# Kernel optimization log

Hardware: AMD Instinct MI355X
Metric: run time of the kernel (lower is better)

Reference implementation:

```python
import jax, jax.numpy as jnp
import numpy as np

N_HEADS = 8
IN_DIM = 128
H_DIM = 512
B, N, L = 4, 64, 256


def setup_inputs() -> dict:
    key = jax.random.key(0)
    ks = jax.random.split(key, 11)
    s = 0.02
    return {
        "query": jax.random.normal(ks[0], (B, N, L, IN_DIM), jnp.float32),
        "key": jax.random.normal(ks[1], (B, N, L, IN_DIM), jnp.float32),
        "value": jax.random.normal(ks[2], (B, N, L, IN_DIM), jnp.float32),
        "Wq": jax.random.normal(ks[3], (IN_DIM, H_DIM), jnp.float32) * s,
        "bq": jnp.zeros((H_DIM,), jnp.float32),
        "Wk": jax.random.normal(ks[4], (IN_DIM, H_DIM), jnp.float32) * s,
        "bk": jnp.zeros((H_DIM,), jnp.float32),
        "Wv": jax.random.normal(ks[5], (IN_DIM, H_DIM), jnp.float32) * s,
        "bv": jnp.zeros((H_DIM,), jnp.float32),
        "Wo": jax.random.normal(ks[6], (H_DIM, H_DIM), jnp.float32) * s,
        "bo": jnp.zeros((H_DIM,), jnp.float32),
    }


def reference(query, key, value, Wq, bq, Wk, bk, Wv, bv, Wo, bo):
    # Conv2d 1x1 over the channel dim after permute == linear along last dim.
    hd = H_DIM // N_HEADS  # head_dim
    b, n, lq, _ = query.shape
    lk = key.shape[-2]
    q = query @ Wq + bq   # (B, N, Lq, H_DIM)
    k = key @ Wk + bk     # (B, N, Lk, H_DIM)
    v = value @ Wv + bv   # (B, N, Lk, H_DIM)
    # split heads along the last dim (matches torch.split/cat head-major trick)
    q = q.reshape(b, n, lq, N_HEADS, hd)
    k = k.reshape(b, n, lk, N_HEADS, hd)
    v = v.reshape(b, n, lk, N_HEADS, hd)
    scores = jnp.einsum("bnqhd,bnkhd->bnhqk", q, k) / jnp.sqrt(jnp.float32(hd))
    attn = jax.nn.softmax(scores, axis=-1)
    out = jnp.einsum("bnhqk,bnkhd->bnqhd", attn, v).reshape(b, n, lq, H_DIM)
    return out @ Wo + bo
```

## Files before the change

### kernel.cpp

```cpp
#include <hip/hip_runtime.h>
#include <stdint.h>
#include <stddef.h>


typedef __attribute__((ext_vector_type(8))) short short8;
typedef __attribute__((ext_vector_type(4))) float f32x4;

#define AS1(p) ((const __attribute__((address_space(1))) void*)(p))
#define AS3(p) ((__attribute__((address_space(3))) void*)(p))

__device__ __forceinline__ float b2f(uint16_t u) {
    union { uint32_t i; float f; } x; x.i = ((uint32_t)u) << 16; return x.f;
}
__device__ __forceinline__ uint16_t f2b(float f) {
    union { float f; uint32_t i; } x; x.f = f;
    uint32_t r = x.i + 0x7fffu + ((x.i >> 16) & 1u);
    return (uint16_t)(r >> 16);
}

__global__ void k_detect(const uint16_t* __restrict__ q, int* __restrict__ flag) {
    const int t = threadIdx.x;
    int cnt = 0;
    for (int i = 0; i < 32; ++i) {
        const int e = (q[t * 32 + i] >> 7) & 0xff;
        cnt += (e < 110) | (e > 135);
    }
#pragma unroll
    for (int m = 1; m < 64; m <<= 1) cnt += __shfl_xor(cnt, m, 64);
    if (t == 0) *flag = (cnt > 256) ? 1 : 0;
}

__device__ __forceinline__ uint16_t rd_any(const void* p, size_t idx, int isf) {
    return isf ? f2b(((const float*)p)[idx]) : ((const uint16_t*)p)[idx];
}

__global__ void k_transpose(const void* __restrict__ Wq, const void* __restrict__ Wk,
                            const void* __restrict__ Wv, const void* __restrict__ Wo,
                            uint16_t* __restrict__ wtq, uint16_t* __restrict__ wtk,
                            uint16_t* __restrict__ wtv, uint16_t* __restrict__ wto,
                            const int* __restrict__ flag) {
    const int isf = *flag;
    const int z = blockIdx.y;
    const int t = blockIdx.x * 256 + threadIdx.x;
    if (z < 3) {
        if (t >= 128 * 512) return;
        const void* W = (z == 0) ? Wq : (z == 1) ? Wk : Wv;
        uint16_t* o = (z == 0) ? wtq : (z == 1) ? wtk : wtv;
        const int k = t & 127, n = t >> 7;
        o[t] = rd_any(W, (size_t)k * 512 + n, isf);
    } else {
        const int k = t & 511, n = t >> 9;
        wto[t] = rd_any(Wo, (size_t)k * 512 + n, isf);
    }
}

template<int KITERS>
__device__ __forceinline__ void gemm_dev(const void* __restrict__ Av, const int lda,
                                         const uint16_t* __restrict__ Wt,
                                         const void* __restrict__ biasv,
                                         void* __restrict__ Cv,
                                         const int m0, const int n0,
                                         const int isf_a, const int isf_bias, const int isf_c) {
    __shared__ __align__(16) uint16_t At[128 * 64];
    __shared__ __align__(16) uint16_t Bt[128 * 64];
    const int tid = threadIdx.x;
    const int lane = tid & 63, w = tid >> 6;
    const int wr = w >> 1, wc = w & 1;
    const int quad = lane >> 4, cl = lane & 15;

    f32x4 acc[4][4];
#pragma unroll
    for (int i = 0; i < 4; ++i)
#pragma unroll
        for (int j = 0; j < 4; ++j) acc[i][j] = (f32x4){0.f, 0.f, 0.f, 0.f};

#pragma unroll 1
    for (int kt = 0; kt < KITERS; ++kt) {
        const int k0 = kt * 64;
        __syncthreads();
        if (!isf_a) {
#pragma unroll
            for (int i = 0; i < 4; ++i) {
                const int s = i * 256 + tid;
                const int row = s >> 3;
                const int gc = (s & 7) ^ (row & 7);
                __builtin_amdgcn_global_load_lds(AS1((const uint16_t*)Av + (size_t)(m0 + row) * lda + k0 + gc * 8),
                                                 AS3(At + (size_t)(i * 256 + w * 64) * 8), 16, 0, 0);
                __builtin_amdgcn_global_load_lds(AS1(Wt + (size_t)(n0 + row) * lda + k0 + gc * 8),
                                                 AS3(Bt + (size_t)(i * 256 + w * 64) * 8), 16, 0, 0);
            }
        } else {
#pragma unroll
            for (int i = 0; i < 4; ++i) {
                const int s = i * 256 + tid;
                const int row = s >> 3;
                const int gc = (s & 7) ^ (row & 7);
                __builtin_amdgcn_global_load_lds(AS1(Wt + (size_t)(n0 + row) * lda + k0 + gc * 8),
                                                 AS3(Bt + (size_t)(i * 256 + w * 64) * 8), 16, 0, 0);
                const float* p = (const float*)Av + (size_t)(m0 + row) * lda + k0 + gc * 8;
                const f32x4 u0 = *(const f32x4*)p;
                const f32x4 u1 = *(const f32x4*)(p + 4);
                short8 tv;
#pragma unroll
                for (int j = 0; j < 4; ++j) {
                    tv[j] = (short)f2b(u0[j]);
                    tv[4 + j] = (short)f2b(u1[j]);
                }
                *(short8*)(At + (size_t)s * 8) = tv;
            }
        }
        __syncthreads();
#pragma unroll
        for (int ks = 0; ks < 2; ++ks) {
            short8 af[4], bf[4];
#pragma unroll
            for (int mt = 0; mt < 4; ++mt) {
                const int row = wr * 64 + mt * 16 + cl;
                const int slot = row * 8 + ((ks * 4 + quad) ^ (row & 7));
                af[mt] = *(const short8*)(At + slot * 8);
            }
#pragma unroll
            for (int nt = 0; nt < 4; ++nt) {
                const int row = wc * 64 + nt * 16 + cl;
                const int slot = row * 8 + ((ks * 4 + quad) ^ (row & 7));
                bf[nt] = *(const short8*)(Bt + slot * 8);
            }
#pragma unroll
            for (int mt = 0; mt < 4; ++mt)
#pragma unroll
                for (int nt = 0; nt < 4; ++nt)
                    acc[mt][nt] = __builtin_amdgcn_mfma_f32_16x16x32_bf16(af[mt], bf[nt], acc[mt][nt], 0, 0, 0);
        }
    }
    if (!isf_c) {
        __syncthreads();
        uint16_t* const Ob = ((w & 2) ? Bt : At) + (w & 1) * 4096;
#pragma unroll
        for (int nt = 0; nt < 4; ++nt) {
            const int col = nt * 16 + cl;
            const float bv = isf_bias ? ((const float*)biasv)[n0 + wc * 64 + col]
                                      : b2f(((const uint16_t*)biasv)[n0 + wc * 64 + col]);
#pragma unroll
            for (int mt = 0; mt < 4; ++mt)
#pragma unroll
                for (int r = 0; r < 4; ++r) {
                    const int row = mt * 16 + quad * 4 + r;
                    Ob[row * 64 + (((col >> 3) ^ (row & 7)) & 7) * 8 + (col & 7)] =
                        f2b(acc[mt][nt][r] + bv);
                }
        }
#pragma unroll
        for (int g = 0; g < 8; ++g) {
            const int row = g * 8 + (lane >> 3);
            const int c = lane & 7;
            const short8 ov = *(const short8*)(Ob + row * 64 + ((c ^ (row & 7)) & 7) * 8);
            *(short8*)((uint16_t*)Cv + (size_t)(m0 + wr * 64 + row) * 512 + n0 + wc * 64 + c * 8) = ov;
        }
    } else {
#pragma unroll
        for (int nt = 0; nt < 4; ++nt) {
            const int col = n0 + wc * 64 + nt * 16 + cl;
            const float bv = isf_bias ? ((const float*)biasv)[col] : b2f(((const uint16_t*)biasv)[col]);
#pragma unroll
            for (int mt = 0; mt < 4; ++mt)
#pragma unroll
                for (int r = 0; r < 4; ++r) {
                    const int rowg = m0 + wr * 64 + mt * 16 + quad * 4 + r;
                    ((float*)Cv)[(size_t)rowg * 512 + col] = acc[mt][nt][r] + bv;
                }
        }
    }
}

__global__ __launch_bounds__(256, 2) void k_gemm_proj(
    const void* qi, const void* ki, const void* vi,
    const uint16_t* wtq, const uint16_t* wtk, const uint16_t* wtv,
    const void* bq, const void* bk, const void* bv,
    uint16_t* cq, uint16_t* ck, uint16_t* cv, const int* flag) {
    const int isf = *flag;
    const int id = blockIdx.x + (blockIdx.y << 2) + (blockIdx.z << 11);
    const int nid = (id & 7) * 768 + (id >> 3);
    const int z = nid >> 11;
    const int y = (nid >> 2) & 511;
    const int x = nid & 3;
    const void* A = (z == 0) ? qi : (z == 1) ? ki : vi;
    const uint16_t* W = (z == 0) ? wtq : (z == 1) ? wtk : wtv;
    const void* B = (z == 0) ? bq : (z == 1) ? bk : bv;
    uint16_t* C = (z == 0) ? cq : (z == 1) ? ck : cv;
    gemm_dev<2>(A, 128, W, B, C, y * 128, x * 128, isf, isf, 0);
}

__global__ __launch_bounds__(256, 2) void k_gemm_out(
    const uint16_t* __restrict__ A, const uint16_t* __restrict__ Wt,
    const void* __restrict__ bias, void* __restrict__ C, const int* flag) {
    const int isf = *flag;
    const int id = blockIdx.x + (blockIdx.y << 2);
    const int nid = (id & 7) * 256 + (id >> 3);
    const int y = nid >> 2;
    const int x = nid & 3;
    gemm_dev<8>(A, 512, Wt, bias, C, y * 128, x * 128, 0, isf, isf);
}

__global__ __launch_bounds__(256, 2) void k_attn(const uint16_t* __restrict__ qws,
                                                 const uint16_t* __restrict__ kws,
                                                 const uint16_t* __restrict__ vws,
                                                 uint16_t* __restrict__ ows) {
    __shared__ __align__(16) uint16_t sm[16384];

    const int bx = blockIdx.x;
    const int bn = bx >> 3, h = bx & 7;
    const int tid = threadIdx.x;
    const int lane = tid & 63, w = tid >> 6;
    const int quad = lane >> 4, cl = lane & 15;
    const size_t base = (size_t)bn * 256 * 512 + h * 64;
    const int qbase = w * 64;

    short8 qf[4][2];
#pragma unroll
    for (int mt = 0; mt < 4; ++mt)
#pragma unroll
        for (int ks = 0; ks < 2; ++ks)
            qf[mt][ks] = *(const short8*)(qws + base + (size_t)(qbase + mt * 16 + cl) * 512 + ks * 32 + quad * 8);

    f32x4 O[4][4];
    float lsum[4];
#pragma unroll
    for (int mt = 0; mt < 4; ++mt) {
#pragma unroll
        for (int nt = 0; nt < 4; ++nt) O[mt][nt] = (f32x4){0.f, 0.f, 0.f, 0.f};
        lsum[mt] = 0.f;
    }

    short8 vreg[2];
    {
#pragma unroll
        for (int i = 0; i < 2; ++i) {
            const int s = i * 256 + tid;
            const int row = s >> 3;
            const int gc = (s & 7) ^ (row & 7);
            __builtin_amdgcn_global_load_lds(AS1(kws + base + (size_t)row * 512 + gc * 8),
                                             AS3(sm + (i * 256 + w * 64) * 8), 16, 0, 0);
        }
#pragma unroll
        for (int i = 0; i < 2; ++i) {
            const int it = i * 256 + tid;
            const int key = it >> 3, db = (it & 7) * 8;
            vreg[i] = *(const short8*)(vws + base + (size_t)key * 512 + db);
        }
#pragma unroll
        for (int i = 0; i < 2; ++i) {
            const int it = i * 256 + tid;
            const int key = it >> 3, db = (it & 7) * 8;
            const int c = ((key >> 5) & 1) * 4 + ((key >> 2) & 3);
            const int j2 = ((key >> 4) & 1) * 4 + (key & 3);
#pragma unroll
            for (int j = 0; j < 8; ++j) {
                const int d = db + j;
                const int fd = ((d >> 3) ^ d) & 7;
                sm[8192 + d * 64 + ((c ^ fd) & 7) * 8 + j2] = (uint16_t)vreg[i][j];
            }
        }
    }
    __syncthreads();

    int cur = 0;
#pragma unroll 1
    for (int kb = 0; kb < 4; ++kb) {
        const uint16_t* const Kc = sm + cur * 4096;
        const uint16_t* const Vc = sm + 8192 + cur * 4096;
        const int nb = cur ^ 1;

        if (kb < 3) {
#pragma unroll
            for (int i = 0; i < 2; ++i) {
                const int s = i * 256 + tid;
                const int row = s >> 3;
                const int gc = (s & 7) ^ (row & 7);
                __builtin_amdgcn_global_load_lds(AS1(kws + base + (size_t)((kb + 1) * 64 + row) * 512 + gc * 8),
                                                 AS3(sm + nb * 4096 + (i * 256 + w * 64) * 8), 16, 0, 0);
            }
#pragma unroll
            for (int i = 0; i < 2; ++i) {
                const int it = i * 256 + tid;
                const int key = it >> 3, db = (it & 7) * 8;
                vreg[i] = *(const short8*)(vws + base + (size_t)((kb + 1) * 64 + key) * 512 + db);
            }
        }

#pragma unroll
        for (int hf = 0; hf < 2; ++hf) {
            short8 kf[2][2];
#pragma unroll
            for (int nt2 = 0; nt2 < 2; ++nt2)
#pragma unroll
                for (int ks = 0; ks < 2; ++ks) {
                    const int row = (hf * 2 + nt2) * 16 + cl;
                    const int slot = row * 8 + ((ks * 4 + quad) ^ (row & 7));
                    kf[nt2][ks] = *(const short8*)(Kc + slot * 8);
                }
            short8 vf[4];
#pragma unroll
            for (int nt = 0; nt < 4; ++nt) {
                const int d = nt * 16 + cl;
                const int fd = ((d >> 3) ^ d) & 7;
                vf[nt] = *(const short8*)(Vc + d * 64 + (((hf * 4 + quad) ^ fd) & 7) * 8);
            }
#pragma unroll
            for (int mt = 0; mt < 4; ++mt) {
                f32x4 S0 = (f32x4){0.f, 0.f, 0.f, 0.f};
                f32x4 S1 = (f32x4){0.f, 0.f, 0.f, 0.f};
#pragma unroll
                for (int ks = 0; ks < 2; ++ks) {
                    S0 = __builtin_amdgcn_mfma_f32_16x16x32_bf16(kf[0][ks], qf[mt][ks], S0, 0, 0, 0);
                    S1 = __builtin_amdgcn_mfma_f32_16x16x32_bf16(kf[1][ks], qf[mt][ks], S1, 0, 0, 0);
                }
                short8 pf;
                float ls = 0.f;
#pragma unroll
                for (int r = 0; r < 4; ++r) {
                    const float pv = __expf(S0[r] * 0.125f);
                    ls += pv;
                    pf[r] = (short)f2b(pv);
                }
#pragma unroll
                for (int r = 0; r < 4; ++r) {
                    const float pv = __expf(S1[r] * 0.125f);
                    ls += pv;
                    pf[4 + r] = (short)f2b(pv);
                }
                lsum[mt] += ls;
#pragma unroll
                for (int nt = 0; nt < 4; ++nt)
                    O[mt][nt] = __builtin_amdgcn_mfma_f32_16x16x32_bf16(pf, vf[nt], O[mt][nt], 0, 0, 0);
            }
        }

        if (kb < 3) {
#pragma unroll
            for (int i = 0; i < 2; ++i) {
                const int it = i * 256 + tid;
                const int key = it >> 3, db = (it & 7) * 8;
                const int c = ((key >> 5) & 1) * 4 + ((key >> 2) & 3);
                const int j2 = ((key >> 4) & 1) * 4 + (key & 3);
#pragma unroll
                for (int j = 0; j < 8; ++j) {
                    const int d = db + j;
                    const int fd = ((d >> 3) ^ d) & 7;
                    sm[8192 + nb * 4096 + d * 64 + ((c ^ fd) & 7) * 8 + j2] = (uint16_t)vreg[i][j];
                }
            }
        }
        __syncthreads();
        cur = nb;
    }

    float linv[4];
#pragma unroll
    for (int mt = 0; mt < 4; ++mt) {
        float v = lsum[mt];
        v += __shfl_xor(v, 16, 64);
        v += __shfl_xor(v, 32, 64);
        linv[mt] = 1.0f / v;
    }

    uint16_t* const Ob = sm + w * 4096;
#pragma unroll
    for (int mt = 0; mt < 4; ++mt) {
        float ln4[4];
#pragma unroll
        for (int r = 0; r < 4; ++r) ln4[r] = __shfl(linv[mt], quad * 4 + r, 64);
#pragma unroll
        for (int nt = 0; nt < 4; ++nt)
#pragma unroll
            for (int r = 0; r < 4; ++r) {
                const int row = mt * 16 + quad * 4 + r;
                const int col = nt * 16 + cl;
                Ob[row * 64 + ((((col >> 3) ^ (row & 7)) & 7) * 8 + (col & 7))] =
                    f2b(O[mt][nt][r] * ln4[r]);
            }
    }
#pragma unroll
    for (int g = 0; g < 8; ++g) {
        const int row = g * 8 + (lane >> 3);
        const int c = lane & 7;
        const short8 ov = *(const short8*)(Ob + row * 64 + ((c ^ (row & 7)) & 7) * 8);
        *(short8*)(ows + base + (size_t)(qbase + row) * 512 + c * 8) = ov;
    }
}

extern "C" void kernel_launch(void* const* d_in, const int* in_sizes, int n_in,
                              void* d_out, int out_size, void* d_ws, size_t ws_size,
                              hipStream_t stream) {
    uint16_t* ws = (uint16_t*)d_ws;

    int* flag = (int*)d_ws;
    uint16_t* wt_q = ws + 256;
    uint16_t* wt_k = wt_q + 128 * 512;
    uint16_t* wt_v = wt_k + 128 * 512;
    uint16_t* wt_o = wt_v + 128 * 512;
    uint16_t* q_ws = wt_o + 512 * 512;
    const size_t QKV = (size_t)65536 * 512;
    uint16_t* k_ws = q_ws + QKV;
    uint16_t* v_ws = k_ws + QKV;

    k_detect<<<1, 64, 0, stream>>>((const uint16_t*)d_in[0], flag);
    k_transpose<<<dim3(1024, 4), 256, 0, stream>>>(d_in[3], d_in[5], d_in[7], d_in[9],
                                                   wt_q, wt_k, wt_v, wt_o, flag);
    k_gemm_proj<<<dim3(4, 512, 3), 256, 0, stream>>>(d_in[0], d_in[1], d_in[2],
                                                     wt_q, wt_k, wt_v,
                                                     d_in[4], d_in[6], d_in[8],
                                                     q_ws, k_ws, v_ws, flag);
    k_attn<<<dim3(2048), 256, 0, stream>>>(q_ws, k_ws, v_ws, q_ws);
    k_gemm_out<<<dim3(4, 512), 256, 0, stream>>>(q_ws, wt_o, d_in[10], d_out, flag);
}
```

Baseline: 428.6 us.

## Load GEMM operand fragments directly from global memory, bypassing LDS staging

The projection GEMM no longer stages A and W tiles through shared memory with async global-to-LDS copies and barriers. Each wave now loads its MFMA fragments straight from global memory into registers, converting fp32 A on the fly. This removes the __syncthreads and LDS round trip but gives up data sharing between waves, so each tile is fetched from global/L2 twice, using more registers and causing more scattered, less coalesced loads.

```diff
diff --git a/kernel.cpp b/kernel.cpp
--- a/kernel.cpp
+++ b/kernel.cpp
@@ -61,8 +61,7 @@
                                          void* __restrict__ Cv,
                                          const int m0, const int n0,
                                          const int isf_a, const int isf_bias, const int isf_c) {
-    __shared__ __align__(16) uint16_t At[128 * 64];
-    __shared__ __align__(16) uint16_t Bt[128 * 64];
+    __shared__ __align__(16) uint16_t Obs[4 * 4096];
     const int tid = threadIdx.x;
     const int lane = tid & 63, w = tid >> 6;
     const int wr = w >> 1, wc = w & 1;
@@ -74,67 +73,59 @@
 #pragma unroll
         for (int j = 0; j < 4; ++j) acc[i][j] = (f32x4){0.f, 0.f, 0.f, 0.f};
 
+    const int arow = m0 + wr * 64 + cl;
+    const int brow = n0 + wc * 64 + cl;
+
 #pragma unroll 1
     for (int kt = 0; kt < KITERS; ++kt) {
-        const int k0 = kt * 64;
-        __syncthreads();
+        const int k0 = kt * 64 + quad * 8;
+        short8 af[4][2], bf[4][2];
         if (!isf_a) {
 #pragma unroll
-            for (int i = 0; i < 4; ++i) {
-                const int s = i * 256 + tid;
-                const int row = s >> 3;
-                const int gc = (s & 7) ^ (row & 7);
-                __builtin_amdgcn_global_load_lds(AS1((const uint16_t*)Av + (size_t)(m0 + row) * lda + k0 + gc * 8),
-                                                 AS3(At + (size_t)(i * 256 + w * 64) * 8), 16, 0, 0);
-                __builtin_amdgcn_global_load_lds(AS1(Wt + (size_t)(n0 + row) * lda + k0 + gc * 8),
-                                                 AS3(Bt + (size_t)(i * 256 + w * 64) * 8), 16, 0, 0);
-            }
+            for (int ks = 0; ks < 2; ++ks)
+#pragma unroll
+                for (int mt = 0; mt < 4; ++mt)
+                    af[mt][ks] = *(const short8*)((const uint16_t*)Av +
+                                 (size_t)(arow + mt * 16) * lda + k0 + ks * 32);
         } else {
-#pragma unroll
-            for (int i = 0; i < 4; ++i) {
-                const int s = i * 256 + tid;
-                const int row = s >> 3;
-                const int gc = (s & 7) ^ (row & 7);
-                __builtin_amdgcn_global_load_lds(AS1(Wt + (size_t)(n0 + row) * lda + k0 + gc * 8),
-                                                 AS3(Bt + (size_t)(i * 256 + w * 64) * 8), 16, 0, 0);
-                const float* p = (const float*)Av + (size_t)(m0 + row) * lda + k0 + gc * 8;
-                const f32x4 u0 = *(const f32x4*)p;
-                const f32x4 u1 = *(const f32x4*)(p + 4);
-                short8 tv;
-#pragma unroll
-                for (int j = 0; j < 4; ++j) {
-                    tv[j] = (short)f2b(u0[j]);
-                    tv[4 + j] = (short)f2b(u1[j]);
-                }
-                *(short8*)(At + (size_t)s * 8) = tv;
-            }
-        }
-        __syncthreads();
-#pragma unroll
-        for (int ks = 0; ks < 2; ++ks) {
-            short8 af[4], bf[4];
-#pragma unroll
-            for (int mt = 0; mt < 4; ++mt) {
-                const int row = wr * 64 + mt * 16 + cl;
-                const int slot = row * 8 + ((ks * 4 + quad) ^ (row & 7));
-                af[mt] = *(const short8*)(At + slot * 8);
-            }
-#pragma unroll
-            for (int nt = 0; nt < 4; ++nt) {
-                const int row = wc * 64 + nt * 16 + cl;
-                const int slot = row * 8 + ((ks * 4 + quad) ^ (row & 7));
-                bf[nt] = *(const short8*)(Bt + slot * 8);
-            }
+            f32x4 u[4][2][2];
+#pragma unroll
+            for (int ks = 0; ks < 2; ++ks)
+#pragma unroll
+                for (int mt = 0; mt < 4; ++mt) {
+                    const float* p = (const float*)Av + (size_t)(arow + mt * 16) * lda + k0 + ks * 32;
+                    u[mt][ks][0] = *(const f32x4*)p;
+                    u[mt][ks][1] = *(const f32x4*)(p + 4);
+                }
+#pragma unroll
+            for (int ks = 0; ks < 2; ++ks)
+#pragma unroll
+                for (int mt = 0; mt < 4; ++mt) {
+                    short8 tv;
+#pragma unroll
+                    for (int j = 0; j < 4; ++j) {
+                        tv[j] = (short)f2b(u[mt][ks][0][j]);
+                        tv[4 + j] = (short)f2b(u[mt][ks][1][j]);
+                    }
+                    af[mt][ks] = tv;
+                }
+        }
+#pragma unroll
+        for (int ks = 0; ks < 2; ++ks)
+#pragma unroll
+            for (int nt = 0; nt < 4; ++nt)
+                bf[nt][ks] = *(const short8*)(Wt + (size_t)(brow + nt * 16) * lda + k0 + ks * 32);
+#pragma unroll
+        for (int ks = 0; ks < 2; ++ks)
 #pragma unroll
             for (int mt = 0; mt < 4; ++mt)
 #pragma unroll
                 for (int nt = 0; nt < 4; ++nt)
-                    acc[mt][nt] = __builtin_amdgcn_mfma_f32_16x16x32_bf16(af[mt], bf[nt], acc[mt][nt], 0, 0, 0);
-        }
-    }
+                    acc[mt][nt] = __builtin_amdgcn_mfma_f32_16x16x32_bf16(af[mt][ks], bf[nt][ks], acc[mt][nt], 0, 0, 0);
+    }
+
     if (!isf_c) {
-        __syncthreads();
-        uint16_t* const Ob = ((w & 2) ? Bt : At) + (w & 1) * 4096;
+        uint16_t* const Ob = Obs + w * 4096;
 #pragma unroll
         for (int nt = 0; nt < 4; ++nt) {
             const int col = nt * 16 + cl;
```

Measured after the change: 538.2 us. 25.6% more time.

## Double-buffer LDS tiles in projection GEMM to overlap loads with MFMA

Applied to the files above, without the earlier changes.

Doubles the shared-memory A/B tiles and restructures the K loop so the next tile is issued into the alternate buffer before computing on the current one, with one barrier per iteration instead of two. The fp32 A path now issues all global loads before converting, which also gives more memory-level parallelism. The goal is to hide global load latency behind MFMA work. In exchange, LDS use doubles to 64KB per block, which can reduce occupancy, and the extra staged registers add pressure.

```diff
diff --git a/kernel.cpp b/kernel.cpp
--- a/kernel.cpp
+++ b/kernel.cpp
@@ -61,8 +61,8 @@
                                          void* __restrict__ Cv,
                                          const int m0, const int n0,
                                          const int isf_a, const int isf_bias, const int isf_c) {
-    __shared__ __align__(16) uint16_t At[128 * 64];
-    __shared__ __align__(16) uint16_t Bt[128 * 64];
+    __shared__ __align__(16) uint16_t At[2 * 128 * 64];
+    __shared__ __align__(16) uint16_t Bt[2 * 128 * 64];
     const int tid = threadIdx.x;
     const int lane = tid & 63, w = tid >> 6;
     const int wr = w >> 1, wc = w & 1;
@@ -74,42 +74,54 @@
 #pragma unroll
         for (int j = 0; j < 4; ++j) acc[i][j] = (f32x4){0.f, 0.f, 0.f, 0.f};
 
-#pragma unroll 1
-    for (int kt = 0; kt < KITERS; ++kt) {
+    auto stage = [&](int kt, int buf) {
         const int k0 = kt * 64;
-        __syncthreads();
-        if (!isf_a) {
+#pragma unroll
+        for (int i = 0; i < 4; ++i) {
+            const int s = i * 256 + tid;
+            const int row = s >> 3;
+            const int gc = (s & 7) ^ (row & 7);
+            __builtin_amdgcn_global_load_lds(AS1(Wt + (size_t)(n0 + row) * lda + k0 + gc * 8),
+                                             AS3(Bt + buf * 8192 + (size_t)(i * 256 + w * 64) * 8), 16, 0, 0);
+            if (!isf_a)
+                __builtin_amdgcn_global_load_lds(AS1((const uint16_t*)Av + (size_t)(m0 + row) * lda + k0 + gc * 8),
+                                                 AS3(At + buf * 8192 + (size_t)(i * 256 + w * 64) * 8), 16, 0, 0);
+        }
+        if (isf_a) {
+            f32x4 u[4][2];
 #pragma unroll
             for (int i = 0; i < 4; ++i) {
                 const int s = i * 256 + tid;
                 const int row = s >> 3;
                 const int gc = (s & 7) ^ (row & 7);
-                __builtin_amdgcn_global_load_lds(AS1((const uint16_t*)Av + (size_t)(m0 + row) * lda + k0 + gc * 8),
-                                                 AS3(At + (size_t)(i * 256 + w * 64) * 8), 16, 0, 0);
-                __builtin_amdgcn_global_load_lds(AS1(Wt + (size_t)(n0 + row) * lda + k0 + gc * 8),
-                                                 AS3(Bt + (size_t)(i * 256 + w * 64) * 8), 16, 0, 0);
-            }
-        } else {
+                const float* p = (const float*)Av + (size_t)(m0 + row) * lda + k0 + gc * 8;
+                u[i][0] = *(const f32x4*)p;
+                u[i][1] = *(const f32x4*)(p + 4);
+            }
 #pragma unroll
             for (int i = 0; i < 4; ++i) {
                 const int s = i * 256 + tid;
-                const int row = s >> 3;
-                const int gc = (s & 7) ^ (row & 7);
-                __builtin_amdgcn_global_load_lds(AS1(Wt + (size_t)(n0 + row) * lda + k0 + gc * 8),
-                                                 AS3(Bt + (size_t)(i * 256 + w * 64) * 8), 16, 0, 0);
-                const float* p = (const float*)Av + (size_t)(m0 + row) * lda + k0 + gc * 8;
-                const f32x4 u0 = *(const f32x4*)p;
-                const f32x4 u1 = *(const f32x4*)(p + 4);
                 short8 tv;
 #pragma unroll
                 for (int j = 0; j < 4; ++j) {
-                    tv[j] = (short)f2b(u0[j]);
-                    tv[4 + j] = (short)f2b(u1[j]);
-                }
-                *(short8*)(At + (size_t)s * 8) = tv;
-            }
-        }
-        __syncthreads();
+                    tv[j] = (short)f2b(u[i][0][j]);
+                    tv[4 + j] = (short)f2b(u[i][1][j]);
+                }
+                *(short8*)(At + buf * 8192 + (size_t)s * 8) = tv;
+            }
+        }
+    };
+
+    stage(0, 0);
+    __syncthreads();
+
+    int cur = 0;
+#pragma unroll 1
+    for (int kt = 0; kt < KITERS; ++kt) {
+        const int nb = cur ^ 1;
+        if (kt + 1 < KITERS) stage(kt + 1, nb);
+        const uint16_t* const Ac = At + cur * 8192;
+        const uint16_t* const Bc = Bt + cur * 8192;
 #pragma unroll
         for (int ks = 0; ks < 2; ++ks) {
             short8 af[4], bf[4];
@@ -117,13 +129,13 @@
             for (int mt = 0; mt < 4; ++mt) {
                 const int row = wr * 64 + mt * 16 + cl;
                 const int slot = row * 8 + ((ks * 4 + quad) ^ (row & 7));
-                af[mt] = *(const short8*)(At + slot * 8);
+                af[mt] = *(const short8*)(Ac + slot * 8);
             }
 #pragma unroll
             for (int nt = 0; nt < 4; ++nt) {
                 const int row = wc * 64 + nt * 16 + cl;
                 const int slot = row * 8 + ((ks * 4 + quad) ^ (row & 7));
-                bf[nt] = *(const short8*)(Bt + slot * 8);
+                bf[nt] = *(const short8*)(Bc + slot * 8);
             }
 #pragma unroll
             for (int mt = 0; mt < 4; ++mt)
@@ -131,10 +143,12 @@
                 for (int nt = 0; nt < 4; ++nt)
                     acc[mt][nt] = __builtin_amdgcn_mfma_f32_16x16x32_bf16(af[mt], bf[nt], acc[mt][nt], 0, 0, 0);
         }
-    }
+        __syncthreads();
+        cur = nb;
+    }
+
     if (!isf_c) {
-        __syncthreads();
-        uint16_t* const Ob = ((w & 2) ? Bt : At) + (w & 1) * 4096;
+        uint16_t* const Ob = At + w * 4096;
 #pragma unroll
         for (int nt = 0; nt < 4; ++nt) {
             const int col = nt * 16 + cl;
```

Result: no change. 425.7 us (-0.7%).
